# Performance work log

Measured on AMD Instinct MI355X. Metric: run time of the kernel, lower is better.

The kernel has to match this reference:

```python
import jax, jax.numpy as jnp
import numpy as np

EMBED_DIM = 1024
HEAD_SIZE = 128
B, S = 8, 2048

def setup_inputs() -> dict:
    rng = jax.random.key(0)
    k1, k2, k3, k4, k5, k6 = jax.random.split(rng, 6)
    std = 1.0 / EMBED_DIM  # nn.initializers.normal(stddev=1/embed_dim)
    return {
        "key": jax.random.normal(k1, (B, S, EMBED_DIM), dtype=jnp.float32),
        "query": jax.random.normal(k2, (B, S, EMBED_DIM), dtype=jnp.float32),
        "value": jax.random.normal(k3, (B, S, EMBED_DIM), dtype=jnp.float32),
        "W_Q": jax.random.normal(k4, (EMBED_DIM, HEAD_SIZE), dtype=jnp.float32) * std,
        "W_K": jax.random.normal(k5, (EMBED_DIM, HEAD_SIZE), dtype=jnp.float32) * std,
        "W_V": jax.random.normal(k6, (EMBED_DIM, HEAD_SIZE), dtype=jnp.float32) * std,
    }

def reference(key, query, value, W_Q, W_K, W_V):
    # Parallel retention: (Q K^T * causal_mask) V
    q_proj = query @ W_Q        # (B, S, H)
    k_proj = key @ W_K          # (B, S, H)
    v_proj = value @ W_V        # (B, S, H)
    ret = jnp.einsum("bsh,bth->bst", q_proj, k_proj)  # (B, S, S)
    # full_self_retention=False -> lower-triangular (causal) mask
    decay_matrix = jnp.tril(jnp.ones((S, S), dtype=ret.dtype))
    ret = ret * decay_matrix
    return ret @ v_proj          # (B, S, H)
```

## Files before the change

### kernel.cpp

```cpp
#include <hip/hip_runtime.h>
#include <cstdint>

#define B_  8
#define S_  2048
#define E_  1024
#define H_  128
#define NC_ 16

typedef __attribute__((ext_vector_type(8))) short bf16x8;
typedef __attribute__((ext_vector_type(4))) float f32x4;

__device__ __forceinline__ short f2bf(float f){
  uint32_t u = __builtin_bit_cast(uint32_t, f);
  u = (u + 0x7fffu + ((u >> 16) & 1u)) >> 16;
  return (short)u;
}
__device__ __forceinline__ float bf2f(short s){
  uint32_t u = ((uint32_t)(uint16_t)s) << 16;
  return __builtin_bit_cast(float, u);
}

__global__ __launch_bounds__(256) void wt_kernel(
    const float* __restrict__ WQ, const float* __restrict__ WK,
    const float* __restrict__ WV,
    short* __restrict__ WtQ, short* __restrict__ WtK, short* __restrict__ WtV)
{
  int which = blockIdx.z;
  const float* W = which == 0 ? WQ : which == 1 ? WK : WV;
  short* Wt      = which == 0 ? WtQ : which == 1 ? WtK : WtV;
  int k0 = blockIdx.x * 32, n0 = blockIdx.y * 32;
  __shared__ float t[32][33];
  int tx = threadIdx.x & 31, ty = threadIdx.x >> 5;
  #pragma unroll
  for (int i = 0; i < 4; i++)
    t[ty + i * 8][tx] = W[(size_t)(k0 + ty + i * 8) * H_ + n0 + tx];
  __syncthreads();
  #pragma unroll
  for (int i = 0; i < 4; i++)
    Wt[(size_t)(n0 + ty + i * 8) * E_ + k0 + tx] = f2bf(t[tx][ty + i * 8]);
}

__global__ __launch_bounds__(256) void proj_kernel(
    const float* __restrict__ Xq, const float* __restrict__ Xk,
    const float* __restrict__ Xv,
    const short* __restrict__ Wtq, const short* __restrict__ Wtk,
    const short* __restrict__ Wtv,
    short* __restrict__ q, short* __restrict__ k,
    short* __restrict__ kT, short* __restrict__ vT)
{
  int which = blockIdx.y;
  const float* X  = which == 0 ? Xq  : which == 1 ? Xk  : Xv;
  const short* Wt = which == 0 ? Wtq : which == 1 ? Wtk : Wtv;

  int tid = threadIdx.x, lane = tid & 63, wave = tid >> 6;
  int lr = lane & 15, lq = lane >> 4;
  int rowbase = blockIdx.x * 64 + wave * 16;

  __shared__ short Bs[128 * 136];

  const float* xr = X + (size_t)(rowbase + lr) * E_ + lq * 8;

  f32x4 acc[8];
  #pragma unroll
  for (int tn = 0; tn < 8; tn++) acc[tn] = (f32x4){0.f, 0.f, 0.f, 0.f};

  for (int kc = 0; kc < 8; kc++){
    if (kc) __syncthreads();
    #pragma unroll
    for (int v = 0; v < 8; v++){
      int c = v * 256 + tid;
      int n = c >> 4, off = (c & 15) * 8;
      *(bf16x8*)(&Bs[n * 136 + off]) =
          *(const bf16x8*)(Wt + (size_t)n * E_ + kc * 128 + off);
    }
    f32x4 ar[8];
    #pragma unroll
    for (int s = 0; s < 4; s++){
      ar[2 * s]     = *(const f32x4*)(xr + kc * 128 + s * 32);
      ar[2 * s + 1] = *(const f32x4*)(xr + kc * 128 + s * 32 + 4);
    }
    __syncthreads();
    #pragma unroll
    for (int s = 0; s < 4; s++){
      bf16x8 a;
      #pragma unroll
      for (int j = 0; j < 4; j++){
        a[j] = f2bf(ar[2 * s][j]); a[4 + j] = f2bf(ar[2 * s + 1][j]);
      }
      #pragma unroll
      for (int tn = 0; tn < 8; tn++){
        bf16x8 bfr = *(const bf16x8*)(&Bs[(tn * 16 + lr) * 136 + s * 32 + lq * 8]);
        acc[tn] = __builtin_amdgcn_mfma_f32_16x16x32_bf16(a, bfr, acc[tn], 0, 0, 0);
      }
    }
  }

  if (which <= 1){
    short* P = which == 0 ? q : k;
    #pragma unroll
    for (int tn = 0; tn < 8; tn++)
      #pragma unroll
      for (int r4 = 0; r4 < 4; r4++)
        P[(size_t)(rowbase + lq * 4 + r4) * H_ + tn * 16 + lr] = f2bf(acc[tn][r4]);
  }
  if (which >= 1){
    short* T = which == 1 ? kT : vT;
    int b = rowbase >> 11, s = rowbase & 2047;
    #pragma unroll
    for (int tn = 0; tn < 8; tn++){
      union { short sh[4]; uint2 u; } pk;
      #pragma unroll
      for (int r4 = 0; r4 < 4; r4++) pk.sh[r4] = f2bf(acc[tn][r4]);
      *(uint2*)(T + ((size_t)b * H_ + tn * 16 + lr) * S_ + s + lq * 4) = pk.u;
    }
  }
}

__global__ __launch_bounds__(256) void chunk_state(
    const short* __restrict__ vT, const short* __restrict__ kT,
    float* __restrict__ M)
{
  int j = blockIdx.x, half = blockIdx.y, b = blockIdx.z;
  int tid = threadIdx.x, lane = tid & 63, wave = tid >> 6;
  int wrow = wave * 32;
  int lr = lane & 15, lq = lane >> 4;

  __shared__ short As[128 * 136];
  __shared__ short Bs[64 * 136];

  const short* vtb = vT + (size_t)b * H_ * S_ + j * 128;
  const short* ktb = kT + (size_t)b * H_ * S_ + (size_t)half * 64 * S_ + j * 128;

  #pragma unroll
  for (int v = 0; v < 8; v++){
    int c = v * 256 + tid;
    int r = c >> 4, off = (c & 15) * 8;
    *(bf16x8*)(&As[r * 136 + off]) = *(const bf16x8*)(vtb + (size_t)r * S_ + off);
  }
  #pragma unroll
  for (int v = 0; v < 4; v++){
    int c = v * 256 + tid;
    int r = c >> 4, off = (c & 15) * 8;
    *(bf16x8*)(&Bs[r * 136 + off]) = *(const bf16x8*)(ktb + (size_t)r * S_ + off);
  }
  __syncthreads();

  f32x4 acc[2][4];
  #pragma unroll
  for (int a = 0; a < 2; a++)
    #pragma unroll
    for (int c = 0; c < 4; c++) acc[a][c] = (f32x4){0.f, 0.f, 0.f, 0.f};

  #pragma unroll
  for (int s = 0; s < 4; s++){
    int t0 = s * 32;
    bf16x8 af[2], bf[4];
    #pragma unroll
    for (int tm = 0; tm < 2; tm++)
      af[tm] = *(const bf16x8*)(&As[(wrow + tm * 16 + lr) * 136 + t0 + lq * 8]);
    #pragma unroll
    for (int tn = 0; tn < 4; tn++)
      bf[tn] = *(const bf16x8*)(&Bs[(tn * 16 + lr) * 136 + t0 + lq * 8]);
    #pragma unroll
    for (int tm = 0; tm < 2; tm++)
      #pragma unroll
      for (int tn = 0; tn < 4; tn++)
        acc[tm][tn] = __builtin_amdgcn_mfma_f32_16x16x32_bf16(
            af[tm], bf[tn], acc[tm][tn], 0, 0, 0);
  }

  float* mb = M + (size_t)(b * NC_ + j) * 16384;
  #pragma unroll
  for (int tm = 0; tm < 2; tm++)
    #pragma unroll
    for (int tn = 0; tn < 4; tn++)
      #pragma unroll
      for (int r4 = 0; r4 < 4; r4++){
        int row = wrow + tm * 16 + lq * 4 + r4;
        int col = half * 64 + tn * 16 + lr;
        mb[row * 128 + col] = acc[tm][tn][r4];
      }
}

__global__ __launch_bounds__(256) void prefix_state(
    const float* __restrict__ M, short* __restrict__ Shi, short* __restrict__ Slo)
{
  int b = blockIdx.y;
  int idx = (blockIdx.x * 256 + threadIdx.x) * 4;
  float4 mv[NC_];
  #pragma unroll
  for (int j = 0; j < NC_; j++)
    mv[j] = *(const float4*)(M + (size_t)(b * NC_ + j) * 16384 + idx);

  float r0 = 0.f, r1 = 0.f, r2 = 0.f, r3 = 0.f;
  #pragma unroll
  for (int j = 0; j < NC_; j++){
    size_t o = (size_t)(b * NC_ + j) * 16384 + idx;
    short h0 = f2bf(r0), h1 = f2bf(r1), h2 = f2bf(r2), h3 = f2bf(r3);
    short l0 = f2bf(r0 - bf2f(h0)), l1 = f2bf(r1 - bf2f(h1));
    short l2 = f2bf(r2 - bf2f(h2)), l3 = f2bf(r3 - bf2f(h3));
    union { short s[4]; uint2 u; } ph, pl;
    ph.s[0] = h0; ph.s[1] = h1; ph.s[2] = h2; ph.s[3] = h3;
    pl.s[0] = l0; pl.s[1] = l1; pl.s[2] = l2; pl.s[3] = l3;
    *(uint2*)(Shi + o) = ph.u;
    *(uint2*)(Slo + o) = pl.u;
    r0 += mv[j].x; r1 += mv[j].y; r2 += mv[j].z; r3 += mv[j].w;
  }
}

__global__ __launch_bounds__(256) void passC(
    const short* __restrict__ qb, const short* __restrict__ kb,
    const short* __restrict__ vT, const short* __restrict__ Shi,
    const short* __restrict__ Slo, float* __restrict__ out)
{
  int i = blockIdx.x, half = blockIdx.y, b = blockIdx.z;
  int roff = half * 64;
  int tid = threadIdx.x, lane = tid & 63, wave = tid >> 6;
  int wrow = (wave >> 1) * 32, wcol = (wave & 1) * 64;
  int lr = lane & 15, lq = lane >> 4;

  __shared__ short Ss[64 * 136];
  __shared__ short Bt[128 * 136];

  const short* qbase = qb + ((size_t)b * S_ + i * 128 + roff) * H_;
  const short* kbase = kb + ((size_t)b * S_ + i * 128) * H_;
  const short* vtb   = vT + (size_t)b * H_ * S_ + i * 128;
  const short* shib  = Shi + (size_t)(b * NC_ + i) * 16384;
  const short* slob  = Slo + (size_t)(b * NC_ + i) * 16384;

  bf16x8 aq[2][4];
  #pragma unroll
  for (int tm = 0; tm < 2; tm++)
    #pragma unroll
    for (int hs = 0; hs < 4; hs++)
      aq[tm][hs] = *(const bf16x8*)(
          qbase + (size_t)(wrow + tm * 16 + lr) * H_ + hs * 32 + lq * 8);

  #pragma unroll
  for (int v = 0; v < 8; v++){
    int c = v * 256 + tid;
    int r = c >> 4, off = (c & 15) * 8;
    *(bf16x8*)(&Bt[r * 136 + off]) = *(const bf16x8*)(kbase + (size_t)r * H_ + off);
  }
  __syncthreads();

  f32x4 acc[2][4];
  #pragma unroll
  for (int a = 0; a < 2; a++)
    #pragma unroll
    for (int c = 0; c < 4; c++) acc[a][c] = (f32x4){0.f, 0.f, 0.f, 0.f};

  #pragma unroll
  for (int hs = 0; hs < 4; hs++){
    bf16x8 bf[4];
    #pragma unroll
    for (int tn = 0; tn < 4; tn++)
      bf[tn] = *(const bf16x8*)(&Bt[(wcol + tn * 16 + lr) * 136 + hs * 32 + lq * 8]);
    #pragma unroll
    for (int tm = 0; tm < 2; tm++)
      #pragma unroll
      for (int tn = 0; tn < 4; tn++)
        acc[tm][tn] = __builtin_amdgcn_mfma_f32_16x16x32_bf16(
            aq[tm][hs], bf[tn], acc[tm][tn], 0, 0, 0);
  }
  __syncthreads();

  #pragma unroll
  for (int tm = 0; tm < 2; tm++)
    #pragma unroll
    for (int tn = 0; tn < 4; tn++)
      #pragma unroll
      for (int r4 = 0; r4 < 4; r4++){
        int row = wrow + tm * 16 + lq * 4 + r4;
        int col = wcol + tn * 16 + lr;
        float vv = (col <= roff + row) ? acc[tm][tn][r4] : 0.f;
        Ss[row * 136 + col] = f2bf(vv);
      }
  #pragma unroll
  for (int v = 0; v < 8; v++){
    int c = v * 256 + tid;
    int r = c >> 4, off = (c & 15) * 8;
    *(bf16x8*)(&Bt[r * 136 + off]) = *(const bf16x8*)(vtb + (size_t)r * S_ + off);
  }
  #pragma unroll
  for (int a = 0; a < 2; a++)
    #pragma unroll
    for (int c = 0; c < 4; c++) acc[a][c] = (f32x4){0.f, 0.f, 0.f, 0.f};
  __syncthreads();

  #pragma unroll
  for (int s = 0; s < 4; s++){
    int t0 = s * 32;
    bf16x8 af[2], bf[4];
    #pragma unroll
    for (int tm = 0; tm < 2; tm++)
      af[tm] = *(const bf16x8*)(&Ss[(wrow + tm * 16 + lr) * 136 + t0 + lq * 8]);
    #pragma unroll
    for (int tn = 0; tn < 4; tn++)
      bf[tn] = *(const bf16x8*)(&Bt[(wcol + tn * 16 + lr) * 136 + t0 + lq * 8]);
    #pragma unroll
    for (int tm = 0; tm < 2; tm++)
      #pragma unroll
      for (int tn = 0; tn < 4; tn++)
        acc[tm][tn] = __builtin_amdgcn_mfma_f32_16x16x32_bf16(
            af[tm], bf[tn], acc[tm][tn], 0, 0, 0);
  }
  __syncthreads();

  #pragma unroll
  for (int part = 0; part < 2; part++){
    const short* sb = part == 0 ? shib : slob;
    #pragma unroll
    for (int v = 0; v < 8; v++){
      int c = v * 256 + tid;
      int r = c >> 4, off = (c & 15) * 8;
      *(bf16x8*)(&Bt[r * 136 + off]) = *(const bf16x8*)(sb + (size_t)r * 128 + off);
    }
    __syncthreads();
    #pragma unroll
    for (int hs = 0; hs < 4; hs++){
      bf16x8 bf[4];
      #pragma unroll
      for (int tn = 0; tn < 4; tn++)
        bf[tn] = *(const bf16x8*)(&Bt[(wcol + tn * 16 + lr) * 136 + hs * 32 + lq * 8]);
      #pragma unroll
      for (int tm = 0; tm < 2; tm++)
        #pragma unroll
        for (int tn = 0; tn < 4; tn++)
          acc[tm][tn] = __builtin_amdgcn_mfma_f32_16x16x32_bf16(
              aq[tm][hs], bf[tn], acc[tm][tn], 0, 0, 0);
    }
    if (part == 0) __syncthreads();
  }

  float* ob = out + ((size_t)b * S_ + i * 128 + roff) * H_;
  #pragma unroll
  for (int tm = 0; tm < 2; tm++)
    #pragma unroll
    for (int tn = 0; tn < 4; tn++)
      #pragma unroll
      for (int r4 = 0; r4 < 4; r4++){
        int row = wrow + tm * 16 + lq * 4 + r4;
        int col = wcol + tn * 16 + lr;
        ob[(size_t)row * H_ + col] = acc[tm][tn][r4];
      }
}

extern "C" void kernel_launch(void* const* d_in, const int* in_sizes, int n_in,
                              void* d_out, int out_size, void* d_ws, size_t ws_size,
                              hipStream_t stream) {
  const float* key   = (const float*)d_in[0];
  const float* query = (const float*)d_in[1];
  const float* value = (const float*)d_in[2];
  const float* WQ    = (const float*)d_in[3];
  const float* WK    = (const float*)d_in[4];
  const float* WV    = (const float*)d_in[5];
  float* out = (float*)d_out;

  char* w = (char*)d_ws;
  short* WtQ = (short*)(w + 0);
  short* WtK = (short*)(w + 262144);
  short* WtV = (short*)(w + 524288);
  size_t o = 786432;
  short* q  = (short*)(w + o); o += 4194304;
  short* k  = (short*)(w + o); o += 4194304;
  short* kT = (short*)(w + o); o += 4194304;
  short* vT = (short*)(w + o); o += 4194304;
  float* M  = (float*)(w + o); o += 8388608;
  short* Shi= (short*)(w + o); o += 4194304;
  short* Slo= (short*)(w + o); o += 4194304;

  wt_kernel   <<<dim3(32, 4, 3),       256, 0, stream>>>(WQ, WK, WV, WtQ, WtK, WtV);
  proj_kernel <<<dim3(256, 3),         256, 0, stream>>>(query, key, value,
                                                         WtQ, WtK, WtV, q, k, kT, vT);
  chunk_state <<<dim3(NC_, 2, B_),     256, 0, stream>>>(vT, kT, M);
  prefix_state<<<dim3(16, B_),         256, 0, stream>>>(M, Shi, Slo);
  passC       <<<dim3(NC_, 2, B_),     256, 0, stream>>>(q, k, vT, Shi, Slo, out);
}
```

Before: 229.1 us.

## Double-buffer projection tiles, prefetch passC operands, widen prefix_state grid

New measurement: 239.2 us. 4.4% more time.

```diff
diff --git a/kernel.cpp b/kernel.cpp
--- a/kernel.cpp
+++ b/kernel.cpp
@@ -56,7 +56,7 @@
   int lr = lane & 15, lq = lane >> 4;
   int rowbase = blockIdx.x * 64 + wave * 16;
 
-  __shared__ short Bs[128 * 136];
+  __shared__ short Bs[2][128 * 72];
 
   const float* xr = X + (size_t)(rowbase + lr) * E_ + lq * 8;
 
@@ -64,34 +64,66 @@
   #pragma unroll
   for (int tn = 0; tn < 8; tn++) acc[tn] = (f32x4){0.f, 0.f, 0.f, 0.f};
 
-  for (int kc = 0; kc < 8; kc++){
-    if (kc) __syncthreads();
-    #pragma unroll
-    for (int v = 0; v < 8; v++){
-      int c = v * 256 + tid;
-      int n = c >> 4, off = (c & 15) * 8;
-      *(bf16x8*)(&Bs[n * 136 + off]) =
-          *(const bf16x8*)(Wt + (size_t)n * E_ + kc * 128 + off);
+  bf16x8 bst[4];
+  f32x4  a0[4], a1[4];
+
+  #pragma unroll
+  for (int v = 0; v < 4; v++){
+    int c = v * 256 + tid;
+    int n = c >> 3, off = (c & 7) * 8;
+    bst[v] = *(const bf16x8*)(Wt + (size_t)n * E_ + off);
+  }
+  #pragma unroll
+  for (int s = 0; s < 2; s++){
+    a0[2 * s]     = *(const f32x4*)(xr + s * 32);
+    a0[2 * s + 1] = *(const f32x4*)(xr + s * 32 + 4);
+  }
+  #pragma unroll
+  for (int v = 0; v < 4; v++){
+    int c = v * 256 + tid;
+    int n = c >> 3, off = (c & 7) * 8;
+    *(bf16x8*)(&Bs[0][n * 72 + off]) = bst[v];
+  }
+  __syncthreads();
+
+  for (int t = 0; t < 16; t++){
+    const int cur = t & 1;
+    if (t < 15){
+      #pragma unroll
+      for (int v = 0; v < 4; v++){
+        int c = v * 256 + tid;
+        int n = c >> 3, off = (c & 7) * 8;
+        bst[v] = *(const bf16x8*)(Wt + (size_t)n * E_ + (t + 1) * 64 + off);
+      }
+      #pragma unroll
+      for (int s = 0; s < 2; s++){
+        a1[2 * s]     = *(const f32x4*)(xr + (t + 1) * 64 + s * 32);
+        a1[2 * s + 1] = *(const f32x4*)(xr + (t + 1) * 64 + s * 32 + 4);
+      }
     }
-    f32x4 ar[8];
-    #pragma unroll
-    for (int s = 0; s < 4; s++){
-      ar[2 * s]     = *(const f32x4*)(xr + kc * 128 + s * 32);
-      ar[2 * s + 1] = *(const f32x4*)(xr + kc * 128 + s * 32 + 4);
+    #pragma unroll
+    for (int s = 0; s < 2; s++){
+      bf16x8 a;
+      #pragma unroll
+      for (int j = 0; j < 4; j++){
+        a[j] = f2bf(a0[2 * s][j]); a[4 + j] = f2bf(a0[2 * s + 1][j]);
+      }
+      #pragma unroll
+      for (int tn = 0; tn < 8; tn++){
+        bf16x8 bfr = *(const bf16x8*)(&Bs[cur][(tn * 16 + lr) * 72 + s * 32 + lq * 8]);
+        acc[tn] = __builtin_amdgcn_mfma_f32_16x16x32_bf16(a, bfr, acc[tn], 0, 0, 0);
+      }
     }
-    __syncthreads();
-    #pragma unroll
-    for (int s = 0; s < 4; s++){
-      bf16x8 a;
-      #pragma unroll
-      for (int j = 0; j < 4; j++){
-        a[j] = f2bf(ar[2 * s][j]); a[4 + j] = f2bf(ar[2 * s + 1][j]);
-      }
-      #pragma unroll
-      for (int tn = 0; tn < 8; tn++){
-        bf16x8 bfr = *(const bf16x8*)(&Bs[(tn * 16 + lr) * 136 + s * 32 + lq * 8]);
-        acc[tn] = __builtin_amdgcn_mfma_f32_16x16x32_bf16(a, bfr, acc[tn], 0, 0, 0);
-      }
+    if (t < 15){
+      #pragma unroll
+      for (int v = 0; v < 4; v++){
+        int c = v * 256 + tid;
+        int n = c >> 3, off = (c & 7) * 8;
+        *(bf16x8*)(&Bs[cur ^ 1][n * 72 + off]) = bst[v];
+      }
+      #pragma unroll
+      for (int i2 = 0; i2 < 4; i2++) a0[i2] = a1[i2];
+      __syncthreads();
     }
   }
 
@@ -105,13 +137,13 @@
   }
   if (which >= 1){
     short* T = which == 1 ? kT : vT;
-    int b = rowbase >> 11, s = rowbase & 2047;
+    int b = rowbase >> 11, srow = rowbase & 2047;
     #pragma unroll
     for (int tn = 0; tn < 8; tn++){
       union { short sh[4]; uint2 u; } pk;
       #pragma unroll
       for (int r4 = 0; r4 < 4; r4++) pk.sh[r4] = f2bf(acc[tn][r4]);
-      *(uint2*)(T + ((size_t)b * H_ + tn * 16 + lr) * S_ + s + lq * 4) = pk.u;
+      *(uint2*)(T + ((size_t)b * H_ + tn * 16 + lr) * S_ + srow + lq * 4) = pk.u;
     }
   }
 }
@@ -186,25 +218,24 @@
     const float* __restrict__ M, short* __restrict__ Shi, short* __restrict__ Slo)
 {
   int b = blockIdx.y;
-  int idx = (blockIdx.x * 256 + threadIdx.x) * 4;
-  float4 mv[NC_];
+  int idx = (blockIdx.x * 256 + threadIdx.x) * 2;
+  float2 mv[NC_];
   #pragma unroll
   for (int j = 0; j < NC_; j++)
-    mv[j] = *(const float4*)(M + (size_t)(b * NC_ + j) * 16384 + idx);
-
-  float r0 = 0.f, r1 = 0.f, r2 = 0.f, r3 = 0.f;
+    mv[j] = *(const float2*)(M + (size_t)(b * NC_ + j) * 16384 + idx);
+
+  float r0 = 0.f, r1 = 0.f;
   #pragma unroll
   for (int j = 0; j < NC_; j++){
     size_t o = (size_t)(b * NC_ + j) * 16384 + idx;
-    short h0 = f2bf(r0), h1 = f2bf(r1), h2 = f2bf(r2), h3 = f2bf(r3);
+    short h0 = f2bf(r0), h1 = f2bf(r1);
     short l0 = f2bf(r0 - bf2f(h0)), l1 = f2bf(r1 - bf2f(h1));
-    short l2 = f2bf(r2 - bf2f(h2)), l3 = f2bf(r3 - bf2f(h3));
-    union { short s[4]; uint2 u; } ph, pl;
-    ph.s[0] = h0; ph.s[1] = h1; ph.s[2] = h2; ph.s[3] = h3;
-    pl.s[0] = l0; pl.s[1] = l1; pl.s[2] = l2; pl.s[3] = l3;
-    *(uint2*)(Shi + o) = ph.u;
-    *(uint2*)(Slo + o) = pl.u;
-    r0 += mv[j].x; r1 += mv[j].y; r2 += mv[j].z; r3 += mv[j].w;
+    union { short s[2]; uint32_t u; } ph, pl;
+    ph.s[0] = h0; ph.s[1] = h1;
+    pl.s[0] = l0; pl.s[1] = l1;
+    *(uint32_t*)(Shi + o) = ph.u;
+    *(uint32_t*)(Slo + o) = pl.u;
+    r0 += mv[j].x; r1 += mv[j].y;
   }
 }
 
@@ -220,7 +251,8 @@
   int lr = lane & 15, lq = lane >> 4;
 
   __shared__ short Ss[64 * 136];
-  __shared__ short Bt[128 * 136];
+  __shared__ short Bt0[128 * 136];
+  __shared__ short Bt1[128 * 136];
 
   const short* qbase = qb + ((size_t)b * S_ + i * 128 + roff) * H_;
   const short* kbase = kb + ((size_t)b * S_ + i * 128) * H_;
@@ -228,6 +260,16 @@
   const short* shib  = Shi + (size_t)(b * NC_ + i) * 16384;
   const short* slob  = Slo + (size_t)(b * NC_ + i) * 16384;
 
+  bf16x8 kst[8], vst[8], hst[8], lst[8];
+  #pragma unroll
+  for (int v = 0; v < 8; v++){
+    int c = v * 256 + tid;
+    int r = c >> 4, off = (c & 15) * 8;
+    kst[v] = *(const bf16x8*)(kbase + (size_t)r * H_ + off);
+    vst[v] = *(const bf16x8*)(vtb  + (size_t)r * S_ + off);
+    hst[v] = *(const bf16x8*)(shib + (size_t)r * 128 + off);
+    lst[v] = *(const bf16x8*)(slob + (size_t)r * 128 + off);
+  }
   bf16x8 aq[2][4];
   #pragma unroll
   for (int tm = 0; tm < 2; tm++)
@@ -240,7 +282,7 @@
   for (int v = 0; v < 8; v++){
     int c = v * 256 + tid;
     int r = c >> 4, off = (c & 15) * 8;
-    *(bf16x8*)(&Bt[r * 136 + off]) = *(const bf16x8*)(kbase + (size_t)r * H_ + off);
+    *(bf16x8*)(&Bt0[r * 136 + off]) = kst[v];
   }
   __syncthreads();
 
@@ -255,7 +297,7 @@
     bf16x8 bf[4];
     #pragma unroll
     for (int tn = 0; tn < 4; tn++)
-      bf[tn] = *(const bf16x8*)(&Bt[(wcol + tn * 16 + lr) * 136 + hs * 32 + lq * 8]);
+      bf[tn] = *(const bf16x8*)(&Bt0[(wcol + tn * 16 + lr) * 136 + hs * 32 + lq * 8]);
     #pragma unroll
     for (int tm = 0; tm < 2; tm++)
       #pragma unroll
@@ -263,7 +305,6 @@
         acc[tm][tn] = __builtin_amdgcn_mfma_f32_16x16x32_bf16(
             aq[tm][hs], bf[tn], acc[tm][tn], 0, 0, 0);
   }
-  __syncthreads();
 
   #pragma unroll
   for (int tm = 0; tm < 2; tm++)
@@ -280,7 +321,7 @@
   for (int v = 0; v < 8; v++){
     int c = v * 256 + tid;
     int r = c >> 4, off = (c & 15) * 8;
-    *(bf16x8*)(&Bt[r * 136 + off]) = *(const bf16x8*)(vtb + (size_t)r * S_ + off);
+    *(bf16x8*)(&Bt1[r * 136 + off]) = vst[v];
   }
   #pragma unroll
   for (int a = 0; a < 2; a++)
@@ -297,7 +338,7 @@
       af[tm] = *(const bf16x8*)(&Ss[(wrow + tm * 16 + lr) * 136 + t0 + lq * 8]);
     #pragma unroll
     for (int tn = 0; tn < 4; tn++)
-      bf[tn] = *(const bf16x8*)(&Bt[(wcol + tn * 16 + lr) * 136 + t0 + lq * 8]);
+      bf[tn] = *(const bf16x8*)(&Bt1[(wcol + tn * 16 + lr) * 136 + t0 + lq * 8]);
     #pragma unroll
     for (int tm = 0; tm < 2; tm++)
       #pragma unroll
@@ -305,32 +346,47 @@
         acc[tm][tn] = __builtin_amdgcn_mfma_f32_16x16x32_bf16(
             af[tm], bf[tn], acc[tm][tn], 0, 0, 0);
   }
-  __syncthreads();
-
-  #pragma unroll
-  for (int part = 0; part < 2; part++){
-    const short* sb = part == 0 ? shib : slob;
-    #pragma unroll
-    for (int v = 0; v < 8; v++){
-      int c = v * 256 + tid;
-      int r = c >> 4, off = (c & 15) * 8;
-      *(bf16x8*)(&Bt[r * 136 + off]) = *(const bf16x8*)(sb + (size_t)r * 128 + off);
-    }
-    __syncthreads();
-    #pragma unroll
-    for (int hs = 0; hs < 4; hs++){
-      bf16x8 bf[4];
+  #pragma unroll
+  for (int v = 0; v < 8; v++){
+    int c = v * 256 + tid;
+    int r = c >> 4, off = (c & 15) * 8;
+    *(bf16x8*)(&Bt0[r * 136 + off]) = hst[v];
+  }
+  __syncthreads();
+
+  #pragma unroll
+  for (int hs = 0; hs < 4; hs++){
+    bf16x8 bf[4];
+    #pragma unroll
+    for (int tn = 0; tn < 4; tn++)
+      bf[tn] = *(const bf16x8*)(&Bt0[(wcol + tn * 16 + lr) * 136 + hs * 32 + lq * 8]);
+    #pragma unroll
+    for (int tm = 0; tm < 2; tm++)
       #pragma unroll
       for (int tn = 0; tn < 4; tn++)
-        bf[tn] = *(const bf16x8*)(&Bt[(wcol + tn * 16 + lr) * 136 + hs * 32 + lq * 8]);
-      #pragma unroll
-      for (int tm = 0; tm < 2; tm++)
-        #pragma unroll
-        for (int tn = 0; tn < 4; tn++)
-          acc[tm][tn] = __builtin_amdgcn_mfma_f32_16x16x32_bf16(
-              aq[tm][hs], bf[tn], acc[tm][tn], 0, 0, 0);
-    }
-    if (part == 0) __syncthreads();
+        acc[tm][tn] = __builtin_amdgcn_mfma_f32_16x16x32_bf16(
+            aq[tm][hs], bf[tn], acc[tm][tn], 0, 0, 0);
+  }
+  #pragma unroll
+  for (int v = 0; v < 8; v++){
+    int c = v * 256 + tid;
+    int r = c >> 4, off = (c & 15) * 8;
+    *(bf16x8*)(&Bt1[r * 136 + off]) = lst[v];
+  }
+  __syncthreads();
+
+  #pragma unroll
+  for (int hs = 0; hs < 4; hs++){
+    bf16x8 bf[4];
+    #pragma unroll
+    for (int tn = 0; tn < 4; tn++)
+      bf[tn] = *(const bf16x8*)(&Bt1[(wcol + tn * 16 + lr) * 136 + hs * 32 + lq * 8]);
+    #pragma unroll
+    for (int tm = 0; tm < 2; tm++)
+      #pragma unroll
+      for (int tn = 0; tn < 4; tn++)
+        acc[tm][tn] = __builtin_amdgcn_mfma_f32_16x16x32_bf16(
+            aq[tm][hs], bf[tn], acc[tm][tn], 0, 0, 0);
   }
 
   float* ob = out + ((size_t)b * S_ + i * 128 + roff) * H_;
@@ -374,6 +430,6 @@
   proj_kernel <<<dim3(256, 3),         256, 0, stream>>>(query, key, value,
                                                          WtQ, WtK, WtV, q, k, kT, vT);
   chunk_state <<<dim3(NC_, 2, B_),     256, 0, stream>>>(vT, kT, M);
-  prefix_state<<<dim3(16, B_),         256, 0, stream>>>(M, Shi, Slo);
+  prefix_state<<<dim3(32, B_),         256, 0, stream>>>(M, Shi, Slo);
   passC       <<<dim3(NC_, 2, B_),     256, 0, stream>>>(q, k, vT, Shi, Slo, out);
 }
```
